# Kernel optimization log

Measured on AMD Instinct MI355X. Metric: run time of the kernel, lower is better.

Reference implementation:

```python
import jax, jax.numpy as jnp
import numpy as np


def setup_inputs() -> dict:
    key = jax.random.key(0)
    ks = jax.random.split(key, 7)
    B, T, D, H = 32, 512, 512, 512
    return {
        "x": jax.random.normal(ks[0], (B, T, D), dtype=jnp.float32),
        "W_Du": jax.random.normal(ks[1], (D, H), dtype=jnp.float32) * (1.0 / np.sqrt(D)),
        "W_Dr1": jax.random.normal(ks[2], (D, H), dtype=jnp.float32) * (1.0 / np.sqrt(D)),
        "W_Dr2": jax.random.normal(ks[3], (D, H), dtype=jnp.float32) * (1.0 / np.sqrt(D)),
        "b_Du": jax.random.normal(ks[4], (H,), dtype=jnp.float32) * 0.02,
        "b_Dr1": jax.random.normal(ks[5], (H,), dtype=jnp.float32) * 0.02,
        "b_Dr2": jax.random.normal(ks[6], (H,), dtype=jnp.float32) * 0.02,
    }


def reference(x, W_Du, W_Dr1, W_Dr2, b_Du, b_Dr1, b_Dr2):
    # Precompute all per-step projections across time (batched matmuls),
    # then run the strictly sequential gated recurrence with lax.scan.
    r1 = jax.nn.softmax(jnp.einsum('btd,dh->bth', x, W_Dr1) + b_Dr1, axis=-1)  # [B,T,H]
    r2 = jax.nn.softmax(jnp.einsum('btd,dh->bth', x, W_Dr2) + b_Dr2, axis=-1)  # [B,T,H]
    u = jnp.tanh(jnp.einsum('btd,dh->bth', x, W_Du) + b_Du)                     # [B,T,H]

    def step(s, inp):
        r1t, r2t, ut = inp
        s_new = r1t * s + r2t * ut
        return s_new, s_new

    init = jnp.zeros((x.shape[0], W_Du.shape[1]), dtype=x.dtype)
    # time-major for scan: [T,B,H]
    _, ys = jax.lax.scan(
        step, init,
        (jnp.swapaxes(r1, 0, 1), jnp.swapaxes(r2, 0, 1), jnp.swapaxes(u, 0, 1)),
    )
    return jnp.swapaxes(ys, 0, 1)  # [B,T,H]
```

## Files before the change

### kernel.cpp

```cpp
#include <hip/hip_runtime.h>
#include <hip/hip_bf16.h>

#define B_N 32
#define T_N 512
#define D_N 512
#define H_N 512
#define M_N (B_N * T_N)

typedef __attribute__((ext_vector_type(8))) short bf16x8;
typedef __attribute__((ext_vector_type(4))) float f32x4;

__device__ __forceinline__ unsigned short f2bf(float f) {
  unsigned u = __float_as_uint(f);
  u += 0x7FFFu + ((u >> 16) & 1u);
  return (unsigned short)(u >> 16);
}
__device__ __forceinline__ unsigned short f2h(float f) {
  _Float16 h = (_Float16)f;
  return *(unsigned short*)&h;
}
__device__ __forceinline__ float h2f(unsigned short u) {
  _Float16 h = *(_Float16*)&u;
  return (float)h;
}

#define GLOAD16(g, l) __builtin_amdgcn_global_load_lds( \
    (const __attribute__((address_space(1))) void*)(g), \
    (__attribute__((address_space(3))) void*)(l), 16, 0, 0)

__global__ void prep_kernel(const float* __restrict__ x,
                            const float* __restrict__ W0,
                            const float* __restrict__ W1,
                            const float* __restrict__ W2,
                            unsigned short* __restrict__ xb,
                            unsigned short* __restrict__ Wt) {
  int blk = blockIdx.x;
  int tid = threadIdx.x;
  if (blk < 768) {
    __shared__ float tile[32][33];
    int id = blk >> 8;
    int t = blk & 255;
    int kr = (t >> 4) << 5;
    int nc = (t & 15) << 5;
    const float* W = (id == 0) ? W0 : (id == 1) ? W1 : W2;
    unsigned short* Wo = Wt + (size_t)id * (D_N * H_N);
    int tx = tid & 31, ty0 = tid >> 5;
    for (int ty = ty0; ty < 32; ty += 8)
      tile[ty][tx] = W[(size_t)(kr + ty) * H_N + nc + tx];
    __syncthreads();
    for (int ty = ty0; ty < 32; ty += 8)
      Wo[(size_t)(nc + ty) * D_N + kr + tx] = f2bf(tile[tx][ty]);
  } else {
    int b = blk - 768;
    const float4* xv = (const float4*)x;
#pragma unroll
    for (int u = 0; u < 4; ++u) {
      int i = b * 1024 + u * 256 + tid;
      float4 v = xv[i];
      ushort4 o;
      o.x = f2bf(v.x); o.y = f2bf(v.y); o.z = f2bf(v.z); o.w = f2bf(v.w);
      ((ushort4*)xb)[i] = o;
    }
  }
}

__global__ void zero_sums(float* __restrict__ S) {
  ((float4*)S)[blockIdx.x * 256 + threadIdx.x] = (float4){0.f, 0.f, 0.f, 0.f};
}

__global__ void inv_sums(float* __restrict__ S) {
  int i = blockIdx.x * 256 + threadIdx.x;
  S[i] = 1.f / S[i];
}

__global__ __launch_bounds__(256) void gemm3(
    const unsigned short* __restrict__ xb,
    const unsigned short* __restrict__ Wt,
    const float* __restrict__ bDu,
    const float* __restrict__ bDr1,
    const float* __restrict__ bDr2,
    unsigned short* __restrict__ uP,
    unsigned short* __restrict__ e1P,
    unsigned short* __restrict__ e2P,
    float* __restrict__ S1,
    float* __restrict__ S2) {
  __shared__ __align__(16) char smem[49152];

  const int tid = threadIdx.x;
  const int lane = tid & 63;
  const int wv = tid >> 6;
  const int wr = wv >> 1;
  const int wc = wv & 1;
  const int g = lane >> 4;
  const int c16 = lane & 15;

  const int m0 = blockIdx.x * 128;
  const int n0 = blockIdx.y * 128;
  const int id = blockIdx.z;
  const unsigned short* Wp = Wt + (size_t)id * (D_N * H_N);

  f32x4 acc[4][4];
#pragma unroll
  for (int mt = 0; mt < 4; ++mt)
#pragma unroll
    for (int nt = 0; nt < 4; ++nt)
      acc[mt][nt] = (f32x4){0.f, 0.f, 0.f, 0.f};

  const int srow = wv * 16 + (lane >> 2);
  const int selem = (lane & 3) * 8;
  const unsigned short* aSrc = xb + (size_t)(m0 + srow) * D_N + selem;
  const unsigned short* bSrc = Wp + (size_t)(n0 + srow) * D_N + selem;
  const int dstOff = wv * 1024;

#define STAGE(ab, kstep) do {                                            \
    const int k0_ = (kstep) * 32;                                        \
    GLOAD16(aSrc + k0_,                 smem + (ab) * 8192 + dstOff);    \
    GLOAD16(aSrc + 64 * D_N + k0_,      smem + (ab) * 8192 + dstOff + 4096); \
    GLOAD16(bSrc + k0_,         smem + 24576 + (ab) * 8192 + dstOff);    \
    GLOAD16(bSrc + 64 * D_N + k0_, smem + 24576 + (ab) * 8192 + dstOff + 4096); \
  } while (0)

#define COMPUTE(ab) do {                                                 \
    bf16x8 af[4], bb[4];                                                 \
    _Pragma("unroll")                                                    \
    for (int mt = 0; mt < 4; ++mt)                                       \
      af[mt] = *(const bf16x8*)(smem + (ab) * 8192 +                     \
                                (wr * 64 + mt * 16 + c16) * 64 + g * 16); \
    _Pragma("unroll")                                                    \
    for (int nt = 0; nt < 4; ++nt)                                       \
      bb[nt] = *(const bf16x8*)(smem + 24576 + (ab) * 8192 +             \
                                (wc * 64 + nt * 16 + c16) * 64 + g * 16); \
    _Pragma("unroll")                                                    \
    for (int mt = 0; mt < 4; ++mt)                                       \
      _Pragma("unroll")                                                  \
      for (int nt = 0; nt < 4; ++nt)                                     \
        acc[mt][nt] = __builtin_amdgcn_mfma_f32_16x16x32_bf16(           \
            af[mt], bb[nt], acc[mt][nt], 0, 0, 0);                       \
  } while (0)

#define WB(n) do {                                                       \
    __builtin_amdgcn_sched_barrier(0);                                   \
    asm volatile("s_waitcnt vmcnt(" #n ")\n\ts_barrier" ::: "memory");   \
    __builtin_amdgcn_sched_barrier(0);                                   \
  } while (0)

  STAGE(0, 0);
  STAGE(1, 1);
#pragma unroll 1
  for (int i = 0; i < 4; ++i) {
    WB(4); STAGE(2, 3 * i + 2); COMPUTE(0);
    WB(4); STAGE(0, 3 * i + 3); COMPUTE(1);
    WB(4); STAGE(1, 3 * i + 4); COMPUTE(2);
  }
  WB(4); STAGE(2, 14); COMPUTE(0);
  WB(4); STAGE(0, 15); COMPUTE(1);
  WB(4); COMPUTE(2);
  WB(0); COMPUTE(0);

  const float* bp = (id == 0) ? bDu : (id == 1) ? bDr1 : bDr2;
  unsigned short* outp = (id == 0) ? uP : (id == 1) ? e1P : e2P;
  float* Sp = (id == 1) ? S1 : S2;
  float bias[4];
#pragma unroll
  for (int nt = 0; nt < 4; ++nt)
    bias[nt] = bp[n0 + wc * 64 + nt * 16 + c16];

#pragma unroll
  for (int mt = 0; mt < 4; ++mt)
#pragma unroll
    for (int i = 0; i < 4; ++i) {
      int row = m0 + wr * 64 + mt * 16 + g * 4 + i;
      unsigned short* op = outp + (size_t)row * H_N + n0 + wc * 64 + c16;
      if (id == 0) {
#pragma unroll
        for (int nt = 0; nt < 4; ++nt) {
          float z = acc[mt][nt][i] + bias[nt];
          float e = __expf(2.f * z);
          op[nt * 16] = f2h(1.f - 2.f * __builtin_amdgcn_rcpf(e + 1.f));
        }
      } else {
        float ps = 0.f;
#pragma unroll
        for (int nt = 0; nt < 4; ++nt) {
          float e = __expf(acc[mt][nt][i] + bias[nt]);
          op[nt * 16] = f2h(e);
          ps += e;
        }
        ps += __shfl_xor(ps, 1);
        ps += __shfl_xor(ps, 2);
        ps += __shfl_xor(ps, 4);
        ps += __shfl_xor(ps, 8);
        if (c16 == 0) atomicAdd(&Sp[row], ps);
      }
    }
#undef STAGE
#undef COMPUTE
#undef WB
}

__global__ void scan_pass1(const unsigned short* __restrict__ e1P,
                           const unsigned short* __restrict__ e2P,
                           const unsigned short* __restrict__ uP,
                           const float* __restrict__ iS1,
                           const float* __restrict__ iS2,
                           float* __restrict__ cP,
                           float* __restrict__ cS) {
  int gt = blockIdx.x * 256 + threadIdx.x;
  int chunk = gt >> 14;
  int r = gt & 16383;
  int b = r >> 9, h = r & 511;
  int row0 = b * T_N + chunk * 64;
  size_t idx = (size_t)row0 * H_N + h;
  float p = 1.f, s = 0.f;
#pragma unroll 4
  for (int j = 0; j < 64; ++j) {
    float a = iS1[row0 + j] * h2f(e1P[idx]);
    float cu = iS2[row0 + j] * h2f(e2P[idx]) * h2f(uP[idx]);
    s = fmaf(a, s, cu);
    p *= a;
    idx += H_N;
  }
  cP[gt] = p;
  cS[gt] = s;
}

__global__ void scan_pass3(const unsigned short* __restrict__ e1P,
                           const unsigned short* __restrict__ e2P,
                           const unsigned short* __restrict__ uP,
                           const float* __restrict__ iS1,
                           const float* __restrict__ iS2,
                           const float* __restrict__ cP,
                           const float* __restrict__ cS,
                           float* __restrict__ out) {
  int gt = blockIdx.x * 256 + threadIdx.x;
  int chunk = gt >> 14;
  int r = gt & 16383;
  int b = r >> 9, h = r & 511;
  float s = 0.f;
  for (int c2 = 0; c2 < chunk; ++c2)
    s = fmaf(cP[c2 * 16384 + r], s, cS[c2 * 16384 + r]);
  int row0 = b * T_N + chunk * 64;
  size_t idx = (size_t)row0 * H_N + h;
#pragma unroll 4
  for (int j = 0; j < 64; ++j) {
    float a = iS1[row0 + j] * h2f(e1P[idx]);
    float cu = iS2[row0 + j] * h2f(e2P[idx]) * h2f(uP[idx]);
    s = fmaf(a, s, cu);
    out[idx] = s;
    idx += H_N;
  }
}

extern "C" void kernel_launch(void* const* d_in, const int* in_sizes, int n_in,
                              void* d_out, int out_size, void* d_ws, size_t ws_size,
                              hipStream_t stream) {
  const float* x  = (const float*)d_in[0];
  const float* W0 = (const float*)d_in[1];
  const float* W1 = (const float*)d_in[2];
  const float* W2 = (const float*)d_in[3];
  const float* b0 = (const float*)d_in[4];
  const float* b1 = (const float*)d_in[5];
  const float* b2 = (const float*)d_in[6];
  float* out = (float*)d_out;

  char* ws = (char*)d_ws;
  unsigned short* xb  = (unsigned short*)ws;
  unsigned short* Wt  = (unsigned short*)(ws + 16777216);
  unsigned short* uP  = (unsigned short*)(ws + 18350080);
  unsigned short* e1P = (unsigned short*)(ws + 35127296);
  unsigned short* e2P = (unsigned short*)(ws + 51904512);
  float*          S1  = (float*)(ws + 68681728);
  float*          S2  = (float*)(ws + 68747264);
  float*          cP  = (float*)(ws + 68812800);
  float*          cS  = (float*)(ws + 69337088);

  zero_sums<<<32, 256, 0, stream>>>(S1);
  prep_kernel<<<2816, 256, 0, stream>>>(x, W0, W1, W2, xb, Wt);
  gemm3<<<dim3(128, 4, 3), 256, 0, stream>>>(xb, Wt, b0, b1, b2,
                                             uP, e1P, e2P, S1, S2);
  inv_sums<<<128, 256, 0, stream>>>(S1);
  scan_pass1<<<512, 256, 0, stream>>>(e1P, e2P, uP, S1, S2, cP, cS);
  scan_pass3<<<512, 256, 0, stream>>>(e1P, e2P, uP, S1, S2, cP, cS, out);
}
```

Before: 90.78 us.

## Fold sum init/inverse into neighbors and widen GEMM K-tile with swizzled LDS

Removes the zero_sums and inv_sums launches: sum zeroing moves into extra blocks of the prep kernel, and the reciprocal of the softmax sums is computed per chunk in shared memory inside both scan kernels. The GEMM now stages 64-wide K tiles into a double-buffered 64 KB LDS region with an XOR swizzle to avoid bank conflicts, with an explicit barrier before overwriting each buffer. This cuts launch overhead and the number of barrier iterations, but doubles LDS use per block, which can lower occupancy, and switches from triple to double buffering.

```diff
diff --git a/kernel.cpp b/kernel.cpp
--- a/kernel.cpp
+++ b/kernel.cpp
@@ -33,7 +33,8 @@
                             const float* __restrict__ W1,
                             const float* __restrict__ W2,
                             unsigned short* __restrict__ xb,
-                            unsigned short* __restrict__ Wt) {
+                            unsigned short* __restrict__ Wt,
+                            float* __restrict__ S) {
   int blk = blockIdx.x;
   int tid = threadIdx.x;
   if (blk < 768) {
@@ -50,7 +51,7 @@
     __syncthreads();
     for (int ty = ty0; ty < 32; ty += 8)
       Wo[(size_t)(nc + ty) * D_N + kr + tx] = f2bf(tile[tx][ty]);
-  } else {
+  } else if (blk < 2816) {
     int b = blk - 768;
     const float4* xv = (const float4*)x;
 #pragma unroll
@@ -61,16 +62,9 @@
       o.x = f2bf(v.x); o.y = f2bf(v.y); o.z = f2bf(v.z); o.w = f2bf(v.w);
       ((ushort4*)xb)[i] = o;
     }
+  } else {
+    ((float4*)S)[(blk - 2816) * 256 + tid] = (float4){0.f, 0.f, 0.f, 0.f};
   }
-}
-
-__global__ void zero_sums(float* __restrict__ S) {
-  ((float4*)S)[blockIdx.x * 256 + threadIdx.x] = (float4){0.f, 0.f, 0.f, 0.f};
-}
-
-__global__ void inv_sums(float* __restrict__ S) {
-  int i = blockIdx.x * 256 + threadIdx.x;
-  S[i] = 1.f / S[i];
 }
 
 __global__ __launch_bounds__(256) void gemm3(
@@ -84,7 +78,7 @@
     unsigned short* __restrict__ e2P,
     float* __restrict__ S1,
     float* __restrict__ S2) {
-  __shared__ __align__(16) char smem[49152];
+  __shared__ __align__(16) char smem[65536];
 
   const int tid = threadIdx.x;
   const int lane = tid & 63;
@@ -106,36 +100,46 @@
     for (int nt = 0; nt < 4; ++nt)
       acc[mt][nt] = (f32x4){0.f, 0.f, 0.f, 0.f};
 
-  const int srow = wv * 16 + (lane >> 2);
-  const int selem = (lane & 3) * 8;
-  const unsigned short* aSrc = xb + (size_t)(m0 + srow) * D_N + selem;
-  const unsigned short* bSrc = Wp + (size_t)(n0 + srow) * D_N + selem;
+  const int rowoff = tid >> 3;
+  const int lsl = ((tid & 7) ^ ((tid >> 3) & 7)) * 8;
+  const unsigned short* aSrc = xb + (size_t)(m0 + rowoff) * D_N + lsl;
+  const unsigned short* bSrc = Wp + (size_t)(n0 + rowoff) * D_N + lsl;
   const int dstOff = wv * 1024;
 
-#define STAGE(ab, kstep) do {                                            \
-    const int k0_ = (kstep) * 32;                                        \
-    GLOAD16(aSrc + k0_,                 smem + (ab) * 8192 + dstOff);    \
-    GLOAD16(aSrc + 64 * D_N + k0_,      smem + (ab) * 8192 + dstOff + 4096); \
-    GLOAD16(bSrc + k0_,         smem + 24576 + (ab) * 8192 + dstOff);    \
-    GLOAD16(bSrc + 64 * D_N + k0_, smem + 24576 + (ab) * 8192 + dstOff + 4096); \
+  const int h3 = c16 & 7;
+
+#define STAGE(buf, kstep) do {                                           \
+    const int k0_ = (kstep) * 64;                                        \
+    _Pragma("unroll")                                                    \
+    for (int i = 0; i < 4; ++i)                                          \
+      GLOAD16(aSrc + (size_t)i * (32 * D_N) + k0_,                       \
+              smem + (buf) * 16384 + dstOff + i * 4096);                 \
+    _Pragma("unroll")                                                    \
+    for (int i = 0; i < 4; ++i)                                          \
+      GLOAD16(bSrc + (size_t)i * (32 * D_N) + k0_,                       \
+              smem + 32768 + (buf) * 16384 + dstOff + i * 4096);         \
   } while (0)
 
-#define COMPUTE(ab) do {                                                 \
-    bf16x8 af[4], bb[4];                                                 \
+#define COMPUTE(buf) do {                                                \
     _Pragma("unroll")                                                    \
-    for (int mt = 0; mt < 4; ++mt)                                       \
-      af[mt] = *(const bf16x8*)(smem + (ab) * 8192 +                     \
-                                (wr * 64 + mt * 16 + c16) * 64 + g * 16); \
-    _Pragma("unroll")                                                    \
-    for (int nt = 0; nt < 4; ++nt)                                       \
-      bb[nt] = *(const bf16x8*)(smem + 24576 + (ab) * 8192 +             \
-                                (wc * 64 + nt * 16 + c16) * 64 + g * 16); \
-    _Pragma("unroll")                                                    \
-    for (int mt = 0; mt < 4; ++mt)                                       \
+    for (int kh = 0; kh < 2; ++kh) {                                     \
+      const int soff = ((kh * 4 + g) ^ h3) << 4;                         \
+      bf16x8 af[4], bb[4];                                               \
+      _Pragma("unroll")                                                  \
+      for (int mt = 0; mt < 4; ++mt)                                     \
+        af[mt] = *(const bf16x8*)(smem + (buf) * 16384 +                 \
+                                  (wr * 64 + mt * 16 + c16) * 128 + soff); \
       _Pragma("unroll")                                                  \
       for (int nt = 0; nt < 4; ++nt)                                     \
-        acc[mt][nt] = __builtin_amdgcn_mfma_f32_16x16x32_bf16(           \
-            af[mt], bb[nt], acc[mt][nt], 0, 0, 0);                       \
+        bb[nt] = *(const bf16x8*)(smem + 32768 + (buf) * 16384 +         \
+                                  (wc * 64 + nt * 16 + c16) * 128 + soff); \
+      _Pragma("unroll")                                                  \
+      for (int mt = 0; mt < 4; ++mt)                                     \
+        _Pragma("unroll")                                                \
+        for (int nt = 0; nt < 4; ++nt)                                   \
+          acc[mt][nt] = __builtin_amdgcn_mfma_f32_16x16x32_bf16(         \
+              af[mt], bb[nt], acc[mt][nt], 0, 0, 0);                     \
+    }                                                                    \
   } while (0)
 
 #define WB(n) do {                                                       \
@@ -144,18 +148,23 @@
     __builtin_amdgcn_sched_barrier(0);                                   \
   } while (0)
 
+#define SB do {                                                          \
+    __builtin_amdgcn_sched_barrier(0);                                   \
+    asm volatile("s_barrier" ::: "memory");                              \
+    __builtin_amdgcn_sched_barrier(0);                                   \
+  } while (0)
+
   STAGE(0, 0);
   STAGE(1, 1);
 #pragma unroll 1
-  for (int i = 0; i < 4; ++i) {
-    WB(4); STAGE(2, 3 * i + 2); COMPUTE(0);
-    WB(4); STAGE(0, 3 * i + 3); COMPUTE(1);
-    WB(4); STAGE(1, 3 * i + 4); COMPUTE(2);
+  for (int t = 0; t < 6; ++t) {
+    WB(8);
+    COMPUTE(t & 1);
+    SB;
+    STAGE(t & 1, t + 2);
   }
-  WB(4); STAGE(2, 14); COMPUTE(0);
-  WB(4); STAGE(0, 15); COMPUTE(1);
-  WB(4); COMPUTE(2);
-  WB(0); COMPUTE(0);
+  WB(8);  COMPUTE(0);
+  WB(0);  COMPUTE(1);
 
   const float* bp = (id == 0) ? bDu : (id == 1) ? bDr1 : bDr2;
   unsigned short* outp = (id == 0) ? uP : (id == 1) ? e1P : e2P;
@@ -196,26 +205,31 @@
 #undef STAGE
 #undef COMPUTE
 #undef WB
+#undef SB
 }
 
 __global__ void scan_pass1(const unsigned short* __restrict__ e1P,
                            const unsigned short* __restrict__ e2P,
                            const unsigned short* __restrict__ uP,
-                           const float* __restrict__ iS1,
-                           const float* __restrict__ iS2,
+                           const float* __restrict__ S1,
+                           const float* __restrict__ S2,
                            float* __restrict__ cP,
                            float* __restrict__ cS) {
+  __shared__ float ls1[64], ls2[64];
   int gt = blockIdx.x * 256 + threadIdx.x;
   int chunk = gt >> 14;
   int r = gt & 16383;
   int b = r >> 9, h = r & 511;
   int row0 = b * T_N + chunk * 64;
+  if (threadIdx.x < 64) ls1[threadIdx.x] = 1.f / S1[row0 + threadIdx.x];
+  else if (threadIdx.x < 128) ls2[threadIdx.x - 64] = 1.f / S2[row0 + threadIdx.x - 64];
+  __syncthreads();
   size_t idx = (size_t)row0 * H_N + h;
   float p = 1.f, s = 0.f;
 #pragma unroll 4
   for (int j = 0; j < 64; ++j) {
-    float a = iS1[row0 + j] * h2f(e1P[idx]);
-    float cu = iS2[row0 + j] * h2f(e2P[idx]) * h2f(uP[idx]);
+    float a = ls1[j] * h2f(e1P[idx]);
+    float cu = ls2[j] * h2f(e2P[idx]) * h2f(uP[idx]);
     s = fmaf(a, s, cu);
     p *= a;
     idx += H_N;
@@ -227,24 +241,28 @@
 __global__ void scan_pass3(const unsigned short* __restrict__ e1P,
                            const unsigned short* __restrict__ e2P,
                            const unsigned short* __restrict__ uP,
-                           const float* __restrict__ iS1,
-                           const float* __restrict__ iS2,
+                           const float* __restrict__ S1,
+                           const float* __restrict__ S2,
                            const float* __restrict__ cP,
                            const float* __restrict__ cS,
                            float* __restrict__ out) {
+  __shared__ float ls1[64], ls2[64];
   int gt = blockIdx.x * 256 + threadIdx.x;
   int chunk = gt >> 14;
   int r = gt & 16383;
   int b = r >> 9, h = r & 511;
+  int row0 = b * T_N + chunk * 64;
+  if (threadIdx.x < 64) ls1[threadIdx.x] = 1.f / S1[row0 + threadIdx.x];
+  else if (threadIdx.x < 128) ls2[threadIdx.x - 64] = 1.f / S2[row0 + threadIdx.x - 64];
   float s = 0.f;
   for (int c2 = 0; c2 < chunk; ++c2)
     s = fmaf(cP[c2 * 16384 + r], s, cS[c2 * 16384 + r]);
-  int row0 = b * T_N + chunk * 64;
+  __syncthreads();
   size_t idx = (size_t)row0 * H_N + h;
 #pragma unroll 4
   for (int j = 0; j < 64; ++j) {
-    float a = iS1[row0 + j] * h2f(e1P[idx]);
-    float cu = iS2[row0 + j] * h2f(e2P[idx]) * h2f(uP[idx]);
+    float a = ls1[j] * h2f(e1P[idx]);
+    float cu = ls2[j] * h2f(e2P[idx]) * h2f(uP[idx]);
     s = fmaf(a, s, cu);
     out[idx] = s;
     idx += H_N;
@@ -274,11 +292,9 @@
   float*          cP  = (float*)(ws + 68812800);
   float*          cS  = (float*)(ws + 69337088);
 
-  zero_sums<<<32, 256, 0, stream>>>(S1);
-  prep_kernel<<<2816, 256, 0, stream>>>(x, W0, W1, W2, xb, Wt);
+  prep_kernel<<<2848, 256, 0, stream>>>(x, W0, W1, W2, xb, Wt, S1);
   gemm3<<<dim3(128, 4, 3), 256, 0, stream>>>(xb, Wt, b0, b1, b2,
                                              uP, e1P, e2P, S1, S2);
-  inv_sums<<<128, 256, 0, stream>>>(S1);
   scan_pass1<<<512, 256, 0, stream>>>(e1P, e2P, uP, S1, S2, cP, cS);
   scan_pass3<<<512, 256, 0, stream>>>(e1P, e2P, uP, S1, S2, cP, cS, out);
 }
```

After: 79.87 us. 12.0% less time.
